# Kernel tuning notes

Hardware: AMD Instinct MI355X
Metric: run time of the kernel (lower is better)

The kernel has to match this reference:

```python
import jax, jax.numpy as jnp
import numpy as np
jax.config.update("jax_enable_x64", True)

B, T, C = 8, 1024, 2048
EXP_K = -6      # power-of-2 exponent of the k/u/w quantization scale (scale = 2**-6)
E_FRAC = 14     # fixed-point fraction bits of the exp LUT
MIN_DELTA = -1024
STEP_I = 1
L_LUT = 1025


def div_rne(x, d):
    # round-to-nearest-even integer division, d > 0 (scalar or array)
    x = x.astype(jnp.int64)
    d = jnp.asarray(d, dtype=jnp.int64)
    sign = jnp.sign(x)
    ax = jnp.abs(x)
    q = ax // d
    r = ax - q * d
    two_r = 2 * r
    inc = (two_r > d) | ((two_r == d) & ((q & 1) == 1))
    return (q + inc.astype(jnp.int64)) * sign


def rshift_rne(x, sh):
    # round-to-nearest-even right shift by static sh > 0
    if sh <= 0:
        return x
    x = x.astype(jnp.int64)
    sign = jnp.sign(x)
    ax = jnp.abs(x)
    half = 1 << (sh - 1)
    mask = (1 << sh) - 1
    r = ax & mask
    q = ax >> sh
    inc = (r > half) | ((r == half) & ((q & 1) == 1))
    return (q + inc.astype(jnp.int64)) * sign


def setup_inputs() -> dict:
    key = jax.random.key(0)
    k1, k2, k3, k4 = jax.random.split(key, 4)
    # per-channel decay (negative) and bonus, at scale 2**EXP_K
    w_i = -jax.random.randint(k1, (C,), 1, 65, dtype=jnp.int32)          # in [-64,-1]
    u_i = jax.random.randint(k2, (C,), -32, 33, dtype=jnp.int32)
    k_i = jax.random.randint(k3, (B, T, C), -2048, 2048, dtype=jnp.int32)
    v_i = jax.random.randint(k4, (B, T, C), -2048, 2048, dtype=jnp.int32)
    # LUT: exp(delta * 2**EXP_K) in Q(e_frac) fixed point, delta in [MIN_DELTA, 0]
    deltas = MIN_DELTA + np.arange(L_LUT) * STEP_I
    lut = np.rint(np.exp(deltas * (2.0 ** EXP_K)) * (1 << E_FRAC)).astype(np.int32)
    return {
        "w_i": w_i, "u_i": u_i, "k_i": k_i, "v_i": v_i,
        "lut": jnp.asarray(lut),
        "min_delta_i": MIN_DELTA, "step_i": STEP_I, "e_frac": E_FRAC,
        "p_bits": 16, "a_bits": 32, "b_bits": 24,
    }


def reference(w_i, u_i, k_i, v_i, lut, min_delta_i, step_i, e_frac, p_bits, a_bits, b_bits):
    # Faithful JAX port of RUN_WKV_INT: integer WKV recurrence with LUT exp,
    # round-to-nearest-even shifts/divides and saturating accumulators.
    Bb, Tt, Cc = k_i.shape
    L = lut.shape[0]
    lut64 = lut.astype(jnp.int64)
    pp0 = -(1 << (p_bits - 1))                    # _qmin_signed(p_bits)
    aa_lo = -(1 << (a_bits - 1))
    aa_hi = (1 << (a_bits - 1)) - 1
    bb_hi = (1 << b_bits) - 1

    def lut_exp(di):  # di <= 0, int64
        num = di.astype(jnp.int64) - min_delta_i
        idx = jnp.clip(div_rne(num, step_i), 0, L - 1)
        return lut64[idx]

    w64 = w_i.astype(jnp.int64)[None, :]   # [1,C]
    u64 = u_i.astype(jnp.int64)[None, :]

    def step(carry, kv):
        pp, aa, bb = carry                 # pp,aa,bb: int64 [B,C]
        kk, vv = kv                        # int64 [B,C]
        # output half-step (includes bonus u)
        ww = kk + u64
        p = jnp.maximum(pp, ww)
        e1 = lut_exp(pp - p)
        e2 = lut_exp(ww - p)
        aa1 = jnp.clip(rshift_rne(aa * e1, e_frac) + vv * e2, aa_lo, aa_hi)
        bb1 = jnp.clip(rshift_rne(bb * e1, e_frac) + e2, 0, bb_hi)
        y = div_rne(aa1, jnp.clip(bb1, 1, bb_hi)).astype(jnp.int32)
        # state half-step (decay w)
        ww2 = pp + w64
        p2 = jnp.maximum(ww2, kk)
        e1n = lut_exp(ww2 - p2)
        e2n = lut_exp(kk - p2)
        aa2 = jnp.clip(rshift_rne(aa1 * e1n, e_frac) + vv * e2n, aa_lo, aa_hi)
        bb2 = jnp.clip(rshift_rne(bb1 * e1n, e_frac) + e2n, 0, bb_hi)
        return (p2, aa2, bb2), y

    init = (
        jnp.full((Bb, Cc), pp0, dtype=jnp.int64),
        jnp.zeros((Bb, Cc), dtype=jnp.int64),
        jnp.zeros((Bb, Cc), dtype=jnp.int64),
    )
    ks = jnp.transpose(k_i, (1, 0, 2)).astype(jnp.int64)  # [T,B,C]
    vs = jnp.transpose(v_i, (1, 0, 2)).astype(jnp.int64)
    _, y = jax.lax.scan(step, init, (ks, vs))
    return jnp.transpose(y, (1, 0, 2))  # [B,T,C] int32
```

## Files before the change

kernel.cpp:

```cpp
#include <hip/hip_runtime.h>
#include <limits.h>


#define TPB 256
#define CC  2048
#define TT  1024
#define TB  16
#define NTB (TT / TB)

static __device__ __forceinline__ int sat_add(int a, int b) {
#if __has_builtin(__builtin_elementwise_add_sat)
    return __builtin_elementwise_add_sat(a, b);
#else
    long long s = (long long)a + (long long)b;
    return s < (long long)INT_MIN ? INT_MIN
         : (s > (long long)INT_MAX ? INT_MAX : (int)s);
#endif
}

static __device__ __forceinline__ int rne14_s(int a, int e) {
    long long x2 = (long long)a * e + 8192;
    int q1 = (int)((unsigned long long)x2 >> 14);
    int tie = (((unsigned)x2 & 32767u) == 16384u);
    return q1 - tie;
}

static __device__ __forceinline__ unsigned rne14_u(unsigned a, unsigned e) {
    unsigned long long x2 = (unsigned long long)a * e + 8192u;
    unsigned q1 = (unsigned)(x2 >> 14);
    unsigned tie = (((unsigned)x2 & 32767u) == 16384u);
    return q1 - tie;
}

__launch_bounds__(TPB, 1)
__global__ void wkv_pipe_kernel(const int* __restrict__ w_i, const int* __restrict__ u_i,
                                const int* __restrict__ k_i, const int* __restrict__ v_i,
                                const int* __restrict__ lut, int* __restrict__ y)
{
    __shared__ int      slut[1025];
    __shared__ int      ering[2][TB][4][64];
    __shared__ int      aaring[2][TB][64];
    __shared__ unsigned ddring[2][TB][64];

    for (int i = threadIdx.x; i < 1025; i += TPB) slut[i] = lut[i];
    __syncthreads();

    const int lane = threadIdx.x & 63;
    const int wid  = threadIdx.x >> 6;
    const int bidx = blockIdx.x;
    const size_t ubase = ((size_t)(bidx >> 5) << 21) + (size_t)((bidx & 31) << 6);

    auto eread = [&](int idx4) -> int {
        idx4 = idx4 < 0 ? 0 : (idx4 > 4096 ? 4096 : idx4);
        return *(const int*)((const char*)slut + idx4);
    };

    if (wid == 0) {
        const int ch = ((bidx & 31) << 6) + lane;
        const int w = w_i[ch], u = u_i[ch];
        const int c1  = 4096 - 4 * u;
        const int c1r = 4096 + 4 * u;
        const int c2  = 4096 + 4 * w;
        const int c2r = 4096 - 4 * w;
        int pp = -32768;
        int kc[TB], kn[TB];
        const int* kb = k_i + ubase;
#pragma unroll
        for (int i = 0; i < TB; ++i) kc[i] = kb[((size_t)i << 11) + lane];
#pragma unroll
        for (int i = 0; i < TB; ++i) kn[i] = kb[((size_t)(TB + i) << 11) + lane];

        for (int j = 0; j < NTB + 2; ++j) {
            if (j < NTB) {
                const int p = j & 1;
#pragma unroll
                for (int i = 0; i < TB; ++i) {
                    const int kk = kc[i];
                    const int s = (pp - kk) << 2;
                    ering[p][i][0][lane] = eread(s + c1);
                    ering[p][i][1][lane] = eread(c1r - s);
                    ering[p][i][2][lane] = eread(s + c2);
                    ering[p][i][3][lane] = eread(c2r - s);
                    const int ppw = pp + w;
                    pp = ppw > kk ? ppw : kk;
                }
#pragma unroll
                for (int i = 0; i < TB; ++i) kc[i] = kn[i];
                if (j + 2 < NTB) {
                    const int* kbn = k_i + ubase + ((size_t)((j + 2) * TB) << 11);
#pragma unroll
                    for (int i = 0; i < TB; ++i) kn[i] = kbn[((size_t)i << 11) + lane];
                }
            }
            __syncthreads();
        }
    } else if (wid == 1) {
        int aa = 0;
        int vc[TB], vn[TB];
        const int* vb = v_i + ubase;
#pragma unroll
        for (int i = 0; i < TB; ++i) vc[i] = vb[((size_t)i << 11) + lane];
#pragma unroll
        for (int i = 0; i < TB; ++i) vn[i] = vb[((size_t)(TB + i) << 11) + lane];

        for (int j = 0; j < NTB + 2; ++j) {
            const int jb = j - 1;
            if (jb >= 0 && jb < NTB) {
                const int p = jb & 1;
#pragma unroll
                for (int i = 0; i < TB; ++i) {
                    const int e1  = ering[p][i][0][lane];
                    const int e2  = ering[p][i][1][lane];
                    const int e1n = ering[p][i][2][lane];
                    const int e2n = ering[p][i][3][lane];
                    const int vv = vc[i];
                    const int aa1 = sat_add(rne14_s(aa, e1), vv * e2);
                    aaring[p][i][lane] = aa1;
                    aa = sat_add(rne14_s(aa1, e1n), vv * e2n);
                }
#pragma unroll
                for (int i = 0; i < TB; ++i) vc[i] = vn[i];
                if (jb + 2 < NTB) {
                    const int* vbn = v_i + ubase + ((size_t)((jb + 2) * TB) << 11);
#pragma unroll
                    for (int i = 0; i < TB; ++i) vn[i] = vbn[((size_t)i << 11) + lane];
                }
            }
            __syncthreads();
        }
    } else if (wid == 2) {
        unsigned bb = 0;
        for (int j = 0; j < NTB + 2; ++j) {
            const int jb = j - 1;
            if (jb >= 0 && jb < NTB) {
                const int p = jb & 1;
#pragma unroll
                for (int i = 0; i < TB; ++i) {
                    const unsigned e1  = (unsigned)ering[p][i][0][lane];
                    const unsigned e2  = (unsigned)ering[p][i][1][lane];
                    const unsigned e1n = (unsigned)ering[p][i][2][lane];
                    const unsigned e2n = (unsigned)ering[p][i][3][lane];
                    unsigned bb1 = rne14_u(bb, e1) + e2;
                    bb1 = bb1 > 0xFFFFFFu ? 0xFFFFFFu : bb1;
                    ddring[p][i][lane] = bb1 > 1u ? bb1 : 1u;
                    unsigned bb2 = rne14_u(bb1, e1n) + e2n;
                    bb = bb2 > 0xFFFFFFu ? 0xFFFFFFu : bb2;
                }
            }
            __syncthreads();
        }
    } else {
        for (int j = 0; j < NTB + 2; ++j) {
            const int jb = j - 2;
            if (jb >= 0) {
                const int p = jb & 1;
                int* yb = y + ubase + ((size_t)(jb * TB) << 11);
#pragma unroll
                for (int i = 0; i < TB; ++i) {
                    const int aa1 = aaring[p][i][lane];
                    const unsigned dd = ddring[p][i][lane];
                    const int sx = aa1 >> 31;
                    const unsigned ua = ((unsigned)aa1 ^ (unsigned)sx) - (unsigned)sx;
                    const unsigned uq = ua / dd;
                    const unsigned ur = ua - uq * dd;
                    const unsigned uy = uq + (unsigned)((2u * ur + (uq & 1u)) > dd);
                    yb[((size_t)i << 11) + lane] = ((int)uy ^ sx) - sx;
                }
            }
            __syncthreads();
        }
    }
}

extern "C" void kernel_launch(void* const* d_in, const int* in_sizes, int n_in,
                              void* d_out, int out_size, void* d_ws, size_t ws_size,
                              hipStream_t stream) {
    const int* w_i = (const int*)d_in[0];
    const int* u_i = (const int*)d_in[1];
    const int* k_i = (const int*)d_in[2];
    const int* v_i = (const int*)d_in[3];
    const int* lut = (const int*)d_in[4];
    int* y = (int*)d_out;
    dim3 grid(8 * CC / 64);
    wkv_pipe_kernel<<<grid, TPB, 0, stream>>>(w_i, u_i, k_i, v_i, lut, y);
}
```

Baseline: 259.7 us.

## Interleave shared-memory rings for vector LDS access and use double rounding divide

Reorders the exp ring so each lane keeps its four LUT factors next to each other, and merges the aa1 and divisor rings into one interleaved int2 ring. Producers now batch their values and write them with 128-bit stores, and consumers prefetch whole blocks with vector loads before the recurrence. The output warp swaps the integer divide-and-round sequence for a double-precision divide plus rint, which matches round-half-even exactly for these magnitudes. The cost is higher register pressure from the batched arrays and possible LDS bank conflicts from the strided int4 layout.

Measured after the change: 255.4 us. About the same (-1.7%).

```diff
diff --git a/kernel.cpp b/kernel.cpp
--- a/kernel.cpp
+++ b/kernel.cpp
@@ -37,10 +37,9 @@
                                 const int* __restrict__ k_i, const int* __restrict__ v_i,
                                 const int* __restrict__ lut, int* __restrict__ y)
 {
-    __shared__ int      slut[1025];
-    __shared__ int      ering[2][TB][4][64];
-    __shared__ int      aaring[2][TB][64];
-    __shared__ unsigned ddring[2][TB][64];
+    __shared__ int slut[1025];
+    __shared__ __align__(16) int ering[2][TB][64][4];
+    __shared__ __align__(16) int yring[2][TB][64][2];
 
     for (int i = threadIdx.x; i < 1025; i += TPB) slut[i] = lut[i];
     __syncthreads();
@@ -73,16 +72,22 @@
         for (int j = 0; j < NTB + 2; ++j) {
             if (j < NTB) {
                 const int p = j & 1;
+                int ea[TB], eb[TB], ec[TB], ed[TB];
 #pragma unroll
                 for (int i = 0; i < TB; ++i) {
                     const int kk = kc[i];
                     const int s = (pp - kk) << 2;
-                    ering[p][i][0][lane] = eread(s + c1);
-                    ering[p][i][1][lane] = eread(c1r - s);
-                    ering[p][i][2][lane] = eread(s + c2);
-                    ering[p][i][3][lane] = eread(c2r - s);
+                    ea[i] = eread(s + c1);
+                    eb[i] = eread(c1r - s);
+                    ec[i] = eread(s + c2);
+                    ed[i] = eread(c2r - s);
                     const int ppw = pp + w;
                     pp = ppw > kk ? ppw : kk;
+                }
+#pragma unroll
+                for (int i = 0; i < TB; ++i) {
+                    int4 t; t.x = ea[i]; t.y = eb[i]; t.z = ec[i]; t.w = ed[i];
+                    *(int4*)&ering[p][i][lane][0] = t;
                 }
 #pragma unroll
                 for (int i = 0; i < TB; ++i) kc[i] = kn[i];
@@ -107,16 +112,16 @@
             const int jb = j - 1;
             if (jb >= 0 && jb < NTB) {
                 const int p = jb & 1;
+                int4 ev[TB];
+#pragma unroll
+                for (int i = 0; i < TB; ++i)
+                    ev[i] = *(const int4*)&ering[p][i][lane][0];
 #pragma unroll
                 for (int i = 0; i < TB; ++i) {
-                    const int e1  = ering[p][i][0][lane];
-                    const int e2  = ering[p][i][1][lane];
-                    const int e1n = ering[p][i][2][lane];
-                    const int e2n = ering[p][i][3][lane];
                     const int vv = vc[i];
-                    const int aa1 = sat_add(rne14_s(aa, e1), vv * e2);
-                    aaring[p][i][lane] = aa1;
-                    aa = sat_add(rne14_s(aa1, e1n), vv * e2n);
+                    const int aa1 = sat_add(rne14_s(aa, ev[i].x), vv * ev[i].y);
+                    yring[p][i][lane][0] = aa1;
+                    aa = sat_add(rne14_s(aa1, ev[i].z), vv * ev[i].w);
                 }
 #pragma unroll
                 for (int i = 0; i < TB; ++i) vc[i] = vn[i];
@@ -134,16 +139,16 @@
             const int jb = j - 1;
             if (jb >= 0 && jb < NTB) {
                 const int p = jb & 1;
+                int4 ev[TB];
+#pragma unroll
+                for (int i = 0; i < TB; ++i)
+                    ev[i] = *(const int4*)&ering[p][i][lane][0];
 #pragma unroll
                 for (int i = 0; i < TB; ++i) {
-                    const unsigned e1  = (unsigned)ering[p][i][0][lane];
-                    const unsigned e2  = (unsigned)ering[p][i][1][lane];
-                    const unsigned e1n = (unsigned)ering[p][i][2][lane];
-                    const unsigned e2n = (unsigned)ering[p][i][3][lane];
-                    unsigned bb1 = rne14_u(bb, e1) + e2;
+                    unsigned bb1 = rne14_u(bb, (unsigned)ev[i].x) + (unsigned)ev[i].y;
                     bb1 = bb1 > 0xFFFFFFu ? 0xFFFFFFu : bb1;
-                    ddring[p][i][lane] = bb1 > 1u ? bb1 : 1u;
-                    unsigned bb2 = rne14_u(bb1, e1n) + e2n;
+                    yring[p][i][lane][1] = (int)(bb1 > 1u ? bb1 : 1u);
+                    unsigned bb2 = rne14_u(bb1, (unsigned)ev[i].z) + (unsigned)ev[i].w;
                     bb = bb2 > 0xFFFFFFu ? 0xFFFFFFu : bb2;
                 }
             }
@@ -155,16 +160,15 @@
             if (jb >= 0) {
                 const int p = jb & 1;
                 int* yb = y + ubase + ((size_t)(jb * TB) << 11);
+                int2 t[TB];
+#pragma unroll
+                for (int i = 0; i < TB; ++i)
+                    t[i] = *(const int2*)&yring[p][i][lane][0];
 #pragma unroll
                 for (int i = 0; i < TB; ++i) {
-                    const int aa1 = aaring[p][i][lane];
-                    const unsigned dd = ddring[p][i][lane];
-                    const int sx = aa1 >> 31;
-                    const unsigned ua = ((unsigned)aa1 ^ (unsigned)sx) - (unsigned)sx;
-                    const unsigned uq = ua / dd;
-                    const unsigned ur = ua - uq * dd;
-                    const unsigned uy = uq + (unsigned)((2u * ur + (uq & 1u)) > dd);
-                    yb[((size_t)i << 11) + lane] = ((int)uy ^ sx) - sx;
+                    const double qa = (double)t[i].x;
+                    const double qd = (double)t[i].y;
+                    yb[((size_t)i << 11) + lane] = (int)rint(qa / qd);
                 }
             }
             __syncthreads();
```
